# Kernel tuning notes

Measured on AMD Instinct MI355X. Metric: run time of the kernel, lower is better.

## Reference

```python
import jax, jax.numpy as jnp
import numpy as np

DZ, DA, K, T, BS, H = 32, 16, 3, 128, 512, 128


def setup_inputs() -> dict:
    key = jax.random.key(0)
    ks = jax.random.split(key, 8)
    s = 0.02
    # A/C: identity-like init (as in the torch module) plus small noise, per mixture k and timestep t
    A = jnp.eye(DZ, dtype=jnp.float32) + s * jax.random.normal(ks[0], (K, T, DZ, DZ), jnp.float32)
    C = jnp.eye(DA, DZ, dtype=jnp.float32) + s * jax.random.normal(ks[1], (K, T, DA, DZ), jnp.float32)
    a0 = jnp.zeros((DA,), jnp.float32)
    a = jax.random.normal(ks[2], (BS, T, DA), jnp.float32)

    def lw(k, shape):
        return 0.05 * jax.random.normal(k, shape, jnp.float32)

    Wih0 = lw(ks[3], (4 * H, DA)); Whh0 = lw(ks[4], (4 * H, H))
    bih0 = jnp.zeros((4 * H,), jnp.float32); bhh0 = jnp.zeros((4 * H,), jnp.float32)
    Wih1 = lw(ks[5], (4 * H, H)); Whh1 = lw(ks[6], (4 * H, H))
    bih1 = jnp.zeros((4 * H,), jnp.float32); bhh1 = jnp.zeros((4 * H,), jnp.float32)
    Wlin = lw(ks[7], (K, H)); blin = jnp.zeros((K,), jnp.float32)
    return dict(a=a, A=A, C=C, a0=a0, Wih0=Wih0, Whh0=Whh0, bih0=bih0, bhh0=bhh0,
                Wih1=Wih1, Whh1=Whh1, bih1=bih1, bhh1=bhh1, Wlin=Wlin, blin=blin)


def _lstm_layer(x, Wih, Whh, bih, bhh):
    # x: (bs, L, din) -> (bs, L, H); PyTorch gate order i, f, g, o; zero initial state
    Hd = Whh.shape[1]
    b = bih + bhh

    def step(carry, xt):
        h, c = carry
        g = xt @ Wih.T + h @ Whh.T + b
        i, f, gg, o = jnp.split(g, 4, axis=-1)
        c = jax.nn.sigmoid(f) * c + jax.nn.sigmoid(i) * jnp.tanh(gg)
        h = jax.nn.sigmoid(o) * jnp.tanh(c)
        return (h, c), h

    h0 = jnp.zeros((x.shape[0], Hd), x.dtype)
    _, hs = jax.lax.scan(step, (h0, h0), jnp.swapaxes(x, 0, 1))
    return jnp.swapaxes(hs, 0, 1)


def _filter(a, A, C, a0, Wih0, Whh0, bih0, bhh0, Wih1, Whh1, bih1, bhh1, Wlin, blin):
    bs, L, da = a.shape
    dz = A.shape[-1]
    R = 0.01 * jnp.eye(da, dtype=a.dtype)
    Q = 0.01 * jnp.eye(dz, dtype=a.dtype)

    # dynamics network: alpha_t from [a_0, a_0..a_{L-2}]
    code = jnp.concatenate([jnp.broadcast_to(a0, (bs, 1, da)), a[:, :-1]], axis=1)
    h = _lstm_layer(code, Wih0, Whh0, bih0, bhh0)
    h = _lstm_layer(h, Wih1, Whh1, bih1, bhh1)
    alpha = jax.nn.softmax(h @ Wlin.T + blin, axis=-1)  # (bs, L, K)

    A_mix = jnp.einsum('blk,klij->blij', alpha, A)  # (bs, L, dz, dz)
    C_mix = jnp.einsum('blk,klij->blij', alpha, C)  # (bs, L, da, dz)
    # A is applied at index t+1 for the prediction step; last slot is a dummy (its output is unused)
    A_next = jnp.concatenate([A_mix[:, 1:], A_mix[:, -1:]], axis=1)

    mu0 = jnp.zeros((bs, dz), a.dtype)
    sig0 = jnp.broadcast_to(jnp.eye(dz, dtype=a.dtype), (bs, dz, dz))
    I = jnp.eye(dz, dtype=a.dtype)

    def step(carry, inp):
        mu_pred, sigma_pred = carry
        Ct, At_next, at = inp  # (bs,da,dz), (bs,dz,dz), (bs,da)
        r = at - jnp.einsum('bij,bj->bi', Ct, mu_pred)
        CtT = jnp.swapaxes(Ct, 1, 2)
        S = Ct @ sigma_pred @ CtT + R                      # (bs, da, da)
        Kg = sigma_pred @ CtT @ jnp.linalg.inv(S)          # (bs, dz, da)
        mu = mu_pred + jnp.einsum('bij,bj->bi', Kg, r)
        sigma = (I - Kg @ Ct) @ sigma_pred
        mu_next = jnp.einsum('bij,bj->bi', At_next, mu)
        sigma_next = At_next @ sigma @ jnp.swapaxes(At_next, 1, 2) + Q
        return (mu_next, sigma_next), mu

    xs = (jnp.swapaxes(C_mix, 0, 1), jnp.swapaxes(A_next, 0, 1), jnp.swapaxes(a, 0, 1))
    _, means = jax.lax.scan(step, (mu0, sig0), xs)
    return jnp.swapaxes(means, 0, 1)  # filtered means (bs, L, dz)


def reference(a, A, C, a0, Wih0, Whh0, bih0, bhh0, Wih1, Whh1, bih1, bhh1, Wlin, blin):
    return _filter(a, A, C, a0, Wih0, Whh0, bih0, bhh0,
                   Wih1, Whh1, bih1, bhh1, Wlin, blin)
```

## Files before the change

kernel.cpp:

```cpp
#include <hip/hip_runtime.h>
#include <hip/hip_fp16.h>
#include <cstdint>

#define T_LEN 128
#define DA    16
#define DZ    32
#define HH    128

__device__ __forceinline__ float sigm(float x){ return 1.0f/(1.0f + __expf(-x)); }
__device__ __forceinline__ float tanh_f(float x){ return 1.0f - 2.0f/(__expf(2.0f*x)+1.0f); }

typedef _Float16 h2v __attribute__((ext_vector_type(2)));
__device__ __forceinline__ float fdot2(uint32_t w, uint32_t h, float acc){
  union{uint32_t u; h2v v;} a, b; a.u = w; b.u = h;
  return __builtin_amdgcn_fdot2(a.v, b.v, acc, false);
}
__device__ __forceinline__ uint32_t packh2(float x, float y){
  return (uint32_t)__half_as_ushort(__float2half(x)) |
         ((uint32_t)__half_as_ushort(__float2half(y)) << 16);
}
__device__ __forceinline__ float h2lo(uint32_t u){
  return __half2float(__ushort_as_half((unsigned short)(u & 0xffffu)));
}
__device__ __forceinline__ float h2hi(uint32_t u){
  return __half2float(__ushort_as_half((unsigned short)(u >> 16)));
}
__device__ __forceinline__ float dot8(uint4 a, uint4 b, float acc){
  acc = fdot2(a.x, b.x, acc); acc = fdot2(a.y, b.y, acc);
  acc = fdot2(a.z, b.z, acc); acc = fdot2(a.w, b.w, acc);
  return acc;
}
__device__ __forceinline__ float dot8f(uint4 h, float4 f0, float4 f1, float acc){
  acc += h2lo(h.x)*f0.x + h2hi(h.x)*f0.y + h2lo(h.y)*f0.z + h2hi(h.y)*f0.w;
  acc += h2lo(h.z)*f1.x + h2hi(h.z)*f1.y + h2lo(h.w)*f1.z + h2hi(h.w)*f1.w;
  return acc;
}

#define BAR() do { asm volatile("s_waitcnt lgkmcnt(0)" ::: "memory"); \
                   __builtin_amdgcn_s_barrier(); } while (0)

__global__ void prep_kernel(const float* __restrict__ Wih0, const float* __restrict__ Whh0,
                            const float* __restrict__ bih0, const float* __restrict__ bhh0,
                            const float* __restrict__ Wih1, const float* __restrict__ Whh1,
                            const float* __restrict__ bih1, const float* __restrict__ bhh1,
                            uint32_t* __restrict__ ws) {
  int idx = blockIdx.x*256 + threadIdx.x;
  if (idx < 4096) {
    int q = idx & 3, g = (idx >> 2) & 511, m = idx >> 11;
    int k0 = 8*m + 2*q;
    ws[idx] = packh2(Wih0[g*DA + k0], Wih0[g*DA + k0 + 1]);
  } else if (idx < 36864) {
    int f = idx - 4096;
    int q = f & 3, g = (f >> 2) & 511, m = f >> 11;
    int k0 = 8*m + 2*q;
    ws[idx] = packh2(Whh0[g*HH + k0], Whh0[g*HH + k0 + 1]);
  } else if (idx < 69632) {
    int f = idx - 36864;
    int q = f & 3, g = (f >> 2) & 511, m = f >> 11;
    int k0 = 8*m + 2*q;
    ws[idx] = packh2(Wih1[g*HH + k0], Wih1[g*HH + k0 + 1]);
  } else if (idx < 102400) {
    int f = idx - 69632;
    int q = f & 3, g = (f >> 2) & 511, m = f >> 11;
    int k0 = 8*m + 2*q;
    ws[idx] = packh2(Whh1[g*HH + k0], Whh1[g*HH + k0 + 1]);
  } else if (idx < 102912) {
    int j = idx - 102400;
    ((float*)ws)[idx] = bih0[j] + bhh0[j];
  } else if (idx < 103424) {
    int j = idx - 102912;
    ((float*)ws)[idx] = bih1[j] + bhh1[j];
  }
}

__global__ __launch_bounds__(512, 2) void lstm_kernel(
    const float* __restrict__ a, const float* __restrict__ a0,
    const uint32_t* __restrict__ wsw, const float* __restrict__ Wlin,
    const float* __restrict__ blin, float* __restrict__ alpha_out) {
  const uint4* Wih0p = (const uint4*)(wsw);
  const uint4* Whh0p = (const uint4*)(wsw + 4096);
  const uint4* Wih1p = (const uint4*)(wsw + 36864);
  const uint4* Whh1p = (const uint4*)(wsw + 69632);
  const float* b0v = (const float*)(wsw + 102400);
  const float* b1v = (const float*)(wsw + 102912);

  __shared__ __align__(16) uint32_t sxh[2][T_LEN][8];
  __shared__ __align__(16) uint32_t sh0h[2][64];
  __shared__ __align__(16) uint32_t sh1h[2][64];
  __shared__ float gates[2][4*HH];
  __shared__ float hpart[4][3];

  int tid = threadIdx.x;
  int lane = tid & 63;
  int wv = tid >> 6;
  int bb = blockIdx.x * 2;

  uint4 wi0[2], wh0[16], wi1[16], wh1[16];
  #pragma unroll
  for (int m = 0; m < 2; ++m)  wi0[m] = Wih0p[m*512 + tid];
  #pragma unroll
  for (int m = 0; m < 16; ++m) wh0[m] = Whh0p[m*512 + tid];
  #pragma unroll
  for (int m = 0; m < 16; ++m) wi1[m] = Wih1p[m*512 + tid];
  #pragma unroll
  for (int m = 0; m < 16; ++m) wh1[m] = Whh1p[m*512 + tid];
  float bi0 = b0v[tid], bi1 = b1v[tid];

  for (int i = tid; i < 2*T_LEN*8; i += 512) {
    int r = i / (T_LEN*8), rem = i % (T_LEN*8), t = rem >> 3, p = rem & 7;
    float x0, x1;
    if (t == 0) { x0 = a0[2*p]; x1 = a0[2*p+1]; }
    else {
      const float* src = a + ((size_t)(bb + r)*T_LEN + (t-1))*DA;
      x0 = src[2*p]; x1 = src[2*p+1];
    }
    sxh[r][t][p] = packh2(x0, x1);
  }
  float wl0 = Wlin[0*HH + (tid & 127)];
  float wl1 = Wlin[1*HH + (tid & 127)];
  float wl2 = Wlin[2*HH + (tid & 127)];
  float bl0 = blin[0], bl1 = blin[1], bl2 = blin[2];
  float cl0 = 0.f, cl1 = 0.f;
  if (tid < 128) { sh0h[wv][lane] = 0u; sh1h[wv][lane] = 0u; }
  __syncthreads();

  #pragma unroll 1
  for (int t = 0; t < T_LEN; ++t) {
    {
      float g0a = bi0, g0b = 0.f, g1a = bi0, g1b = 0.f;
      uint4 xA0 = *(const uint4*)&sxh[0][t][0];
      uint4 xA1 = *(const uint4*)&sxh[0][t][4];
      uint4 xB0 = *(const uint4*)&sxh[1][t][0];
      uint4 xB1 = *(const uint4*)&sxh[1][t][4];
      g0a = fdot2(wi0[0].x, xA0.x, g0a); g0b = fdot2(wi0[0].y, xA0.y, g0b);
      g0a = fdot2(wi0[0].z, xA0.z, g0a); g0b = fdot2(wi0[0].w, xA0.w, g0b);
      g0a = fdot2(wi0[1].x, xA1.x, g0a); g0b = fdot2(wi0[1].y, xA1.y, g0b);
      g0a = fdot2(wi0[1].z, xA1.z, g0a); g0b = fdot2(wi0[1].w, xA1.w, g0b);
      g1a = fdot2(wi0[0].x, xB0.x, g1a); g1b = fdot2(wi0[0].y, xB0.y, g1b);
      g1a = fdot2(wi0[0].z, xB0.z, g1a); g1b = fdot2(wi0[0].w, xB0.w, g1b);
      g1a = fdot2(wi0[1].x, xB1.x, g1a); g1b = fdot2(wi0[1].y, xB1.y, g1b);
      g1a = fdot2(wi0[1].z, xB1.z, g1a); g1b = fdot2(wi0[1].w, xB1.w, g1b);
      #pragma unroll
      for (int m = 0; m < 16; ++m) {
        uint4 w = wh0[m];
        uint4 hA = *(const uint4*)&sh0h[0][4*m];
        uint4 hB = *(const uint4*)&sh0h[1][4*m];
        g0a = fdot2(w.x, hA.x, g0a); g0b = fdot2(w.y, hA.y, g0b);
        g0a = fdot2(w.z, hA.z, g0a); g0b = fdot2(w.w, hA.w, g0b);
        g1a = fdot2(w.x, hB.x, g1a); g1b = fdot2(w.y, hB.y, g1b);
        g1a = fdot2(w.z, hB.z, g1a); g1b = fdot2(w.w, hB.w, g1b);
      }
      gates[0][tid] = g0a + g0b;
      gates[1][tid] = g1a + g1b;
    }
    __syncthreads();
    if (t > 0 && tid >= 504 && tid < 506) {
      int row = tid - 504;
      float l0 = hpart[2*row][0] + hpart[2*row+1][0] + bl0;
      float l1 = hpart[2*row][1] + hpart[2*row+1][1] + bl1;
      float l2 = hpart[2*row][2] + hpart[2*row+1][2] + bl2;
      float mx = fmaxf(l0, fmaxf(l1, l2));
      float e0=__expf(l0-mx), e1=__expf(l1-mx), e2=__expf(l2-mx);
      float inv = 1.0f/(e0+e1+e2);
      float* dst = alpha_out + (((size_t)(bb+row))*T_LEN + (t-1))*3;
      dst[0]=e0*inv; dst[1]=e1*inv; dst[2]=e2*inv;
    }
    if (tid < 256) {
      int row = tid >> 7, cell = tid & 127;
      float iv = gates[row][cell],      fv = gates[row][cell+HH],
            qv = gates[row][cell+2*HH], ov = gates[row][cell+3*HH];
      cl0 = sigm(fv)*cl0 + sigm(iv)*tanh_f(qv);
      float hv = sigm(ov)*tanh_f(cl0);
      ((__half*)&sh0h[0][0])[row*128 + cell] = __float2half(hv);
    }
    __syncthreads();
    {
      float g0a = bi1, g0b = 0.f, g1a = bi1, g1b = 0.f;
      #pragma unroll
      for (int m = 0; m < 16; ++m) {
        uint4 w = wi1[m];
        uint4 hA = *(const uint4*)&sh0h[0][4*m];
        uint4 hB = *(const uint4*)&sh0h[1][4*m];
        g0a = fdot2(w.x, hA.x, g0a); g0b = fdot2(w.y, hA.y, g0b);
        g0a = fdot2(w.z, hA.z, g0a); g0b = fdot2(w.w, hA.w, g0b);
        g1a = fdot2(w.x, hB.x, g1a); g1b = fdot2(w.y, hB.y, g1b);
        g1a = fdot2(w.z, hB.z, g1a); g1b = fdot2(w.w, hB.w, g1b);
      }
      #pragma unroll
      for (int m = 0; m < 16; ++m) {
        uint4 w = wh1[m];
        uint4 hA = *(const uint4*)&sh1h[0][4*m];
        uint4 hB = *(const uint4*)&sh1h[1][4*m];
        g0a = fdot2(w.x, hA.x, g0a); g0b = fdot2(w.y, hA.y, g0b);
        g0a = fdot2(w.z, hA.z, g0a); g0b = fdot2(w.w, hA.w, g0b);
        g1a = fdot2(w.x, hB.x, g1a); g1b = fdot2(w.y, hB.y, g1b);
        g1a = fdot2(w.z, hB.z, g1a); g1b = fdot2(w.w, hB.w, g1b);
      }
      gates[0][tid] = g0a + g0b;
      gates[1][tid] = g1a + g1b;
    }
    __syncthreads();
    if (tid < 256) {
      int row = tid >> 7, cell = tid & 127;
      float iv = gates[row][cell],      fv = gates[row][cell+HH],
            qv = gates[row][cell+2*HH], ov = gates[row][cell+3*HH];
      cl1 = sigm(fv)*cl1 + sigm(iv)*tanh_f(qv);
      float hv = sigm(ov)*tanh_f(cl1);
      ((__half*)&sh1h[0][0])[row*128 + cell] = __float2half(hv);
      float p0 = hv*wl0, p1 = hv*wl1, p2 = hv*wl2;
      #pragma unroll
      for (int off = 32; off > 0; off >>= 1) {
        p0 += __shfl_down(p0, off); p1 += __shfl_down(p1, off); p2 += __shfl_down(p2, off);
      }
      if (lane == 0) {
        int w4 = tid >> 6;
        hpart[w4][0] = p0; hpart[w4][1] = p1; hpart[w4][2] = p2;
      }
    }
  }
  __syncthreads();
  if (tid >= 504 && tid < 506) {
    int row = tid - 504;
    float l0 = hpart[2*row][0] + hpart[2*row+1][0] + bl0;
    float l1 = hpart[2*row][1] + hpart[2*row+1][1] + bl1;
    float l2 = hpart[2*row][2] + hpart[2*row+1][2] + bl2;
    float mx = fmaxf(l0, fmaxf(l1, l2));
    float e0=__expf(l0-mx), e1=__expf(l1-mx), e2=__expf(l2-mx);
    float inv = 1.0f/(e0+e1+e2);
    float* dst = alpha_out + (((size_t)(bb+row))*T_LEN + (T_LEN-1))*3;
    dst[0]=e0*inv; dst[1]=e1*inv; dst[2]=e2*inv;
  }
}

__global__ __launch_bounds__(256) void kalman_kernel(
    const float* __restrict__ a, const float* __restrict__ A,
    const float* __restrict__ C, const float* __restrict__ alpha,
    float* __restrict__ out) {
  __shared__ __align__(16) uint32_t SgH[DZ][20];
  __shared__ __align__(16) uint32_t AmH[2][DZ][20];
  __shared__ __align__(16) uint32_t CmH[2][DA][20];
  __shared__ __align__(16) uint32_t Sp2H[DZ][20];
  __shared__ __align__(16) uint32_t T2H[DZ][20];
  __shared__ __align__(16) uint32_t NnTH[DA][20];
  __shared__ __align__(16) uint32_t NnH[DZ][12];
  __shared__ __align__(16) uint32_t KgH[DZ][12];
  __shared__ __align__(16) uint32_t SinvH[DA][12];
  __shared__ __align__(16) float Aug[DA][36];
  __shared__ __align__(16) float sa[T_LEN][DA];
  __shared__ float salpha[T_LEN*3];
  __shared__ __align__(16) float muvF[DZ], munF[DZ], rv[DA];

  int tid = threadIdx.x;
  int b = blockIdx.x;

  for (int e = tid; e < T_LEN*DA; e += 256) (&sa[0][0])[e] = a[(size_t)b*T_LEN*DA + e];
  for (int e = tid; e < T_LEN*3; e += 256) salpha[e] = alpha[(size_t)b*T_LEN*3 + e];
  __syncthreads();

  const int i8 = tid >> 3, jq = tid & 7;
  const int i32 = tid & 31, g = tid >> 5;
  const int j2 = g * 2, j4 = g * 4;

  {
    uint2 iv;
    iv.x = packh2((i8==4*jq  )?1.f:0.f, (i8==4*jq+1)?1.f:0.f);
    iv.y = packh2((i8==4*jq+2)?1.f:0.f, (i8==4*jq+3)?1.f:0.f);
    *(uint2*)&SgH[i8][jq*2] = iv;
    if (tid < DZ) muvF[tid] = 0.0f;
  }

  const float4* A4 = (const float4*)A;
  const float4* C4 = (const float4*)C;
  float4 pA0 = A4[(0*T_LEN + 1)*256 + tid];
  float4 pA1 = A4[(1*T_LEN + 1)*256 + tid];
  float4 pA2 = A4[(2*T_LEN + 1)*256 + tid];
  float4 pC0, pC1, pC2;
  if (tid < 128) {
    pC0 = C4[(0*T_LEN + 0)*128 + tid];
    pC1 = C4[(1*T_LEN + 0)*128 + tid];
    pC2 = C4[(2*T_LEN + 0)*128 + tid];
  }
  #define MIX_AND_PREFETCH(bf, s, sn)                                          \
  {                                                                            \
    int ta_ = ((s) < T_LEN-1) ? (s)+1 : (s);                                   \
    float bA0 = salpha[ta_*3+0], bA1 = salpha[ta_*3+1], bA2 = salpha[ta_*3+2]; \
    float bC0 = salpha[(s)*3+0], bC1 = salpha[(s)*3+1], bC2 = salpha[(s)*3+2]; \
    float vx = bA0*pA0.x + bA1*pA1.x + bA2*pA2.x;                              \
    float vy = bA0*pA0.y + bA1*pA1.y + bA2*pA2.y;                              \
    float vz = bA0*pA0.z + bA1*pA1.z + bA2*pA2.z;                              \
    float vw = bA0*pA0.w + bA1*pA1.w + bA2*pA2.w;                              \
    uint2 pv; pv.x = packh2(vx, vy); pv.y = packh2(vz, vw);                    \
    *(uint2*)&AmH[bf][i8][jq*2] = pv;                                          \
    if (tid < 128) {                                                           \
      float cx = bC0*pC0.x + bC1*pC1.x + bC2*pC2.x;                            \
      float cy = bC0*pC0.y + bC1*pC1.y + bC2*pC2.y;                            \
      float cz = bC0*pC0.z + bC1*pC1.z + bC2*pC2.z;                            \
      float cw = bC0*pC0.w + bC1*pC1.w + bC2*pC2.w;                            \
      uint2 pc; pc.x = packh2(cx, cy); pc.y = packh2(cz, cw);                  \
      *(uint2*)&CmH[bf][tid>>3][(tid&7)*2] = pc;                               \
    }                                                                          \
    int sn_ = ((sn) < T_LEN) ? (sn) : T_LEN-1;                                 \
    int tan_ = (sn_ < T_LEN-1) ? sn_+1 : sn_;                                  \
    pA0 = A4[(0*T_LEN + tan_)*256 + tid];                                      \
    pA1 = A4[(1*T_LEN + tan_)*256 + tid];                                      \
    pA2 = A4[(2*T_LEN + tan_)*256 + tid];                                      \
    if (tid < 128) {                                                           \
      pC0 = C4[(0*T_LEN + sn_)*128 + tid];                                     \
      pC1 = C4[(1*T_LEN + sn_)*128 + tid];                                     \
      pC2 = C4[(2*T_LEN + sn_)*128 + tid];                                     \
    }                                                                          \
  }

  MIX_AND_PREFETCH(0, 0, 1)
  __syncthreads();

  #pragma unroll 1
  for (int t = 0; t < T_LEN; ++t) {
    const int p = t & 1;

    {
      uint4 s0 = *(const uint4*)&SgH[i32][0];
      uint4 s1 = *(const uint4*)&SgH[i32][4];
      uint4 s2 = *(const uint4*)&SgH[i32][8];
      uint4 s3 = *(const uint4*)&SgH[i32][12];
      uint4 cA0 = *(const uint4*)&CmH[p][j2][0];
      uint4 cA1 = *(const uint4*)&CmH[p][j2][4];
      uint4 cA2 = *(const uint4*)&CmH[p][j2][8];
      uint4 cA3 = *(const uint4*)&CmH[p][j2][12];
      uint4 cB0 = *(const uint4*)&CmH[p][j2+1][0];
      uint4 cB1 = *(const uint4*)&CmH[p][j2+1][4];
      uint4 cB2 = *(const uint4*)&CmH[p][j2+1][8];
      uint4 cB3 = *(const uint4*)&CmH[p][j2+1][12];
      float aA = dot8(s3,cA3, dot8(s2,cA2, dot8(s1,cA1, dot8(s0,cA0, 0.f))));
      float aB = dot8(s3,cB3, dot8(s2,cB2, dot8(s1,cB1, dot8(s0,cB0, 0.f))));
      NnH[i32][g] = packh2(aA, aB);
      __half* ntp = (__half*)&NnTH[0][0];
      ntp[j2*40 + i32]     = __float2half(aA);
      ntp[(j2+1)*40 + i32] = __float2half(aB);
    }
    BAR();

    {
      int i = tid & 15, j = tid >> 4;
      uint4 c0 = *(const uint4*)&CmH[p][i][0];
      uint4 c1 = *(const uint4*)&CmH[p][i][4];
      uint4 c2 = *(const uint4*)&CmH[p][i][8];
      uint4 c3 = *(const uint4*)&CmH[p][i][12];
      uint4 n0 = *(const uint4*)&NnTH[j][0];
      uint4 n1 = *(const uint4*)&NnTH[j][4];
      uint4 n2 = *(const uint4*)&NnTH[j][8];
      uint4 n3 = *(const uint4*)&NnTH[j][12];
      float s = dot8(c3,n3, dot8(c2,n2, dot8(c1,n1, dot8(c0,n0, 0.f))));
      Aug[i][j] = s + ((i == j) ? 0.01f : 0.0f);
      Aug[i][16 + j] = (i == j) ? 1.0f : 0.0f;
    }
    BAR();

    if (tid < 64) {
      int lane = tid;
      int r = lane >> 2, cb = lane & 3;
      float v[8];
      #pragma unroll
      for (int j = 0; j < 8; ++j) v[j] = Aug[r][cb*8 + j];
      #define GJ_PIVOT(P, CTRL)                                                \
      {                                                                        \
        float App = __int_as_float(__builtin_amdgcn_readlane(                  \
                      __float_as_int(v[(P) & 7]), ((P) << 2) | ((P) >> 3)));   \
        float fv  = __int_as_float(__builtin_amdgcn_mov_dpp(                   \
                      __float_as_int(v[(P) & 7]), (CTRL), 0xf, 0xf, true));    \
        float prow[8];                                                         \
        _Pragma("unroll")                                                      \
        for (int j = 0; j < 8; ++j) prow[j] = __shfl(v[j], ((P) << 2) | cb, 64); \
        float pinv = 1.0f / App;                                               \
        if (r == (P)) {                                                        \
          _Pragma("unroll")                                                    \
          for (int j = 0; j < 8; ++j) v[j] *= pinv;                            \
        } else {                                                               \
          float fp = fv * pinv;                                                \
          _Pragma("unroll")                                                    \
          for (int j = 0; j < 8; ++j) v[j] -= fp * prow[j];                    \
        }                                                                      \
      }
      GJ_PIVOT(0, 0x00)  GJ_PIVOT(1, 0x00)  GJ_PIVOT(2, 0x00)  GJ_PIVOT(3, 0x00)
      GJ_PIVOT(4, 0x00)  GJ_PIVOT(5, 0x00)  GJ_PIVOT(6, 0x00)  GJ_PIVOT(7, 0x00)
      GJ_PIVOT(8, 0x55)  GJ_PIVOT(9, 0x55)  GJ_PIVOT(10, 0x55) GJ_PIVOT(11, 0x55)
      GJ_PIVOT(12, 0x55) GJ_PIVOT(13, 0x55) GJ_PIVOT(14, 0x55) GJ_PIVOT(15, 0x55)
      #undef GJ_PIVOT
      if (cb >= 2) {
        uint4 w;
        w.x = packh2(v[0], v[1]); w.y = packh2(v[2], v[3]);
        w.z = packh2(v[4], v[5]); w.w = packh2(v[6], v[7]);
        *(uint4*)&SinvH[r][(cb-2)*4] = w;
      }
    } else if (tid < 64 + DA) {
      int j = tid - 64;
      uint4 c0 = *(const uint4*)&CmH[p][j][0];
      uint4 c1 = *(const uint4*)&CmH[p][j][4];
      uint4 c2 = *(const uint4*)&CmH[p][j][8];
      uint4 c3 = *(const uint4*)&CmH[p][j][12];
      const float4* mv = (const float4*)muvF;
      float4 m0 = mv[0], m1 = mv[1], m2 = mv[2], m3 = mv[3];
      float4 m4 = mv[4], m5 = mv[5], m6 = mv[6], m7 = mv[7];
      float d = 0.f;
      d = dot8f(c0, m0, m1, d);
      d = dot8f(c1, m2, m3, d);
      d = dot8f(c2, m4, m5, d);
      d = dot8f(c3, m6, m7, d);
      rv[j] = sa[t][j] - d;
    }
    BAR();

    {
      uint4 n0 = *(const uint4*)&NnH[i32][0];
      uint4 n1 = *(const uint4*)&NnH[i32][4];
      uint4 sA0 = *(const uint4*)&SinvH[j2][0];
      uint4 sA1 = *(const uint4*)&SinvH[j2][4];
      uint4 sB0 = *(const uint4*)&SinvH[j2+1][0];
      uint4 sB1 = *(const uint4*)&SinvH[j2+1][4];
      float aA = dot8(n1, sA1, dot8(n0, sA0, 0.f));
      float aB = dot8(n1, sB1, dot8(n0, sB0, 0.f));
      KgH[i32][g] = packh2(aA, aB);
    }
    BAR();

    {
      uint4 k0 = *(const uint4*)&KgH[i32][0];
      uint4 k1 = *(const uint4*)&KgH[i32][4];
      float acc[4];
      #pragma unroll
      for (int c = 0; c < 4; ++c) {
        uint4 b0 = *(const uint4*)&NnH[j4+c][0];
        uint4 b1 = *(const uint4*)&NnH[j4+c][4];
        acc[c] = dot8(k1, b1, dot8(k0, b0, 0.f));
      }
      uint2 sgp = *(const uint2*)&SgH[i32][g*2];
      uint2 o;
      o.x = packh2(h2lo(sgp.x) - acc[0], h2hi(sgp.x) - acc[1]);
      o.y = packh2(h2lo(sgp.y) - acc[2], h2hi(sgp.y) - acc[3]);
      *(uint2*)&Sp2H[i32][g*2] = o;
    }
    if (tid >= 128 && tid < 128 + DZ) {
      int q = tid - 128;
      uint4 k0 = *(const uint4*)&KgH[q][0];
      uint4 k1 = *(const uint4*)&KgH[q][4];
      const float4* rp = (const float4*)rv;
      float4 r0 = rp[0], r1 = rp[1], r2 = rp[2], r3 = rp[3];
      float m = muvF[q];
      m = dot8f(k0, r0, r1, m);
      m = dot8f(k1, r2, r3, m);
      munF[q] = m;
      out[((size_t)b*T_LEN + t)*DZ + q] = m;
    }
    BAR();

    {
      uint4 a0 = *(const uint4*)&AmH[p][i32][0];
      uint4 a1 = *(const uint4*)&AmH[p][i32][4];
      uint4 a2 = *(const uint4*)&AmH[p][i32][8];
      uint4 a3 = *(const uint4*)&AmH[p][i32][12];
      float acc[4];
      #pragma unroll
      for (int c = 0; c < 4; ++c) {
        uint4 p0 = *(const uint4*)&Sp2H[j4+c][0];
        uint4 p1 = *(const uint4*)&Sp2H[j4+c][4];
        uint4 p2 = *(const uint4*)&Sp2H[j4+c][8];
        uint4 p3 = *(const uint4*)&Sp2H[j4+c][12];
        acc[c] = dot8(a3,p3, dot8(a2,p2, dot8(a1,p1, dot8(a0,p0, 0.f))));
      }
      uint2 o; o.x = packh2(acc[0], acc[1]); o.y = packh2(acc[2], acc[3]);
      *(uint2*)&T2H[i32][g*2] = o;
    }
    BAR();

    {
      uint4 t0 = *(const uint4*)&T2H[i32][0];
      uint4 t1 = *(const uint4*)&T2H[i32][4];
      uint4 t2 = *(const uint4*)&T2H[i32][8];
      uint4 t3 = *(const uint4*)&T2H[i32][12];
      float acc[4];
      #pragma unroll
      for (int c = 0; c < 4; ++c) {
        uint4 a0 = *(const uint4*)&AmH[p][j4+c][0];
        uint4 a1 = *(const uint4*)&AmH[p][j4+c][4];
        uint4 a2 = *(const uint4*)&AmH[p][j4+c][8];
        uint4 a3 = *(const uint4*)&AmH[p][j4+c][12];
        acc[c] = dot8(t3,a3, dot8(t2,a2, dot8(t1,a1, dot8(t0,a0, 0.f))));
        if (i32 == j4 + c) acc[c] += 0.01f;
      }
      uint2 o; o.x = packh2(acc[0], acc[1]); o.y = packh2(acc[2], acc[3]);
      *(uint2*)&SgH[i32][g*2] = o;
    }
    if (tid >= 128 && tid < 128 + DZ) {
      int q = tid - 128;
      uint4 a0 = *(const uint4*)&AmH[p][q][0];
      uint4 a1 = *(const uint4*)&AmH[p][q][4];
      uint4 a2 = *(const uint4*)&AmH[p][q][8];
      uint4 a3 = *(const uint4*)&AmH[p][q][12];
      const float4* mp = (const float4*)munF;
      float4 n0 = mp[0], n1 = mp[1], n2 = mp[2], n3 = mp[3];
      float4 n4 = mp[4], n5 = mp[5], n6 = mp[6], n7 = mp[7];
      float m = 0.f;
      m = dot8f(a0, n0, n1, m);
      m = dot8f(a1, n2, n3, m);
      m = dot8f(a2, n4, n5, m);
      m = dot8f(a3, n6, n7, m);
      muvF[q] = m;
    }
    {
      int s = (t+1 < T_LEN) ? t+1 : T_LEN-1;
      MIX_AND_PREFETCH(p^1, s, t+2)
    }
    BAR();
  }
  #undef MIX_AND_PREFETCH
}

extern "C" void kernel_launch(void* const* d_in, const int* in_sizes, int n_in,
                              void* d_out, int out_size, void* d_ws, size_t ws_size,
                              hipStream_t stream) {
  const float* a    = (const float*)d_in[0];
  const float* A    = (const float*)d_in[1];
  const float* C    = (const float*)d_in[2];
  const float* a0   = (const float*)d_in[3];
  const float* Wih0 = (const float*)d_in[4];
  const float* Whh0 = (const float*)d_in[5];
  const float* bih0 = (const float*)d_in[6];
  const float* bhh0 = (const float*)d_in[7];
  const float* Wih1 = (const float*)d_in[8];
  const float* Whh1 = (const float*)d_in[9];
  const float* bih1 = (const float*)d_in[10];
  const float* bhh1 = (const float*)d_in[11];
  const float* Wlin = (const float*)d_in[12];
  const float* blin = (const float*)d_in[13];
  uint32_t* ws = (uint32_t*)d_ws;
  float* alpha = (float*)(ws + 103424);
  float* out = (float*)d_out;

  prep_kernel<<<404, 256, 0, stream>>>(Wih0, Whh0, bih0, bhh0, Wih1, Whh1, bih1, bhh1, ws);
  lstm_kernel<<<256, 512, 0, stream>>>(a, a0, ws, Wlin, blin, alpha);
  kalman_kernel<<<512, 256, 0, stream>>>(a, A, C, alpha, out);
}
```

Before: 1.048 ms.

## Solve S·[Kᵀ|w]=[Nᵀ|r] directly via Gauss-Jordan instead of explicit inverse

```diff
diff --git a/kernel.cpp b/kernel.cpp
--- a/kernel.cpp
+++ b/kernel.cpp
@@ -244,11 +244,10 @@
   __shared__ __align__(16) uint32_t NnTH[DA][20];
   __shared__ __align__(16) uint32_t NnH[DZ][12];
   __shared__ __align__(16) uint32_t KgH[DZ][12];
-  __shared__ __align__(16) uint32_t SinvH[DA][12];
-  __shared__ __align__(16) float Aug[DA][36];
+  __shared__ __align__(16) float Aug[DA][20];
   __shared__ __align__(16) float sa[T_LEN][DA];
   __shared__ float salpha[T_LEN*3];
-  __shared__ __align__(16) float muvF[DZ], munF[DZ], rv[DA];
+  __shared__ __align__(16) float muvF[DZ], munF[DZ], rv[DA], wvF[DA];
 
   int tid = threadIdx.x;
   int b = blockIdx.x;
@@ -337,6 +336,20 @@
       __half* ntp = (__half*)&NnTH[0][0];
       ntp[j2*40 + i32]     = __float2half(aA);
       ntp[(j2+1)*40 + i32] = __float2half(aB);
+      if (tid >= 192 && tid < 192 + DA) {
+        int jr = tid - 192;
+        uint4 d0 = *(const uint4*)&CmH[p][jr][0];
+        uint4 d1 = *(const uint4*)&CmH[p][jr][4];
+        uint4 d2 = *(const uint4*)&CmH[p][jr][8];
+        uint4 d3 = *(const uint4*)&CmH[p][jr][12];
+        const float4* mv = (const float4*)muvF;
+        float d = 0.f;
+        d = dot8f(d0, mv[0], mv[1], d);
+        d = dot8f(d1, mv[2], mv[3], d);
+        d = dot8f(d2, mv[4], mv[5], d);
+        d = dot8f(d3, mv[6], mv[7], d);
+        rv[jr] = sa[t][jr] - d;
+      }
     }
     BAR();
 
@@ -352,74 +365,57 @@
       uint4 n3 = *(const uint4*)&NnTH[j][12];
       float s = dot8(c3,n3, dot8(c2,n2, dot8(c1,n1, dot8(c0,n0, 0.f))));
       Aug[i][j] = s + ((i == j) ? 0.01f : 0.0f);
-      Aug[i][16 + j] = (i == j) ? 1.0f : 0.0f;
     }
     BAR();
 
     if (tid < 64) {
       int lane = tid;
       int r = lane >> 2, cb = lane & 3;
-      float v[8];
-      #pragma unroll
-      for (int j = 0; j < 8; ++j) v[j] = Aug[r][cb*8 + j];
-      #define GJ_PIVOT(P, CTRL)                                                \
+      int base = cb * 13;
+      const __half* ntrow = (const __half*)&NnTH[r][0];
+      float v[13];
+      #pragma unroll
+      for (int k = 0; k < 13; ++k) {
+        int c = base + k;
+        float x = 0.f;
+        if (c < 16) x = Aug[r][c];
+        else if (c < 48) x = __half2float(ntrow[c - 16]);
+        else if (c == 48) x = rv[r];
+        v[k] = x;
+      }
+      #define GJS_PIVOT(P, E, CTRL)                                            \
       {                                                                        \
         float App = __int_as_float(__builtin_amdgcn_readlane(                  \
-                      __float_as_int(v[(P) & 7]), ((P) << 2) | ((P) >> 3)));   \
+                      __float_as_int(v[(E)]), ((P) << 2) | ((P) / 13)));       \
         float fv  = __int_as_float(__builtin_amdgcn_mov_dpp(                   \
-                      __float_as_int(v[(P) & 7]), (CTRL), 0xf, 0xf, true));    \
-        float prow[8];                                                         \
+                      __float_as_int(v[(E)]), (CTRL), 0xf, 0xf, true));        \
+        float prow[13];                                                        \
         _Pragma("unroll")                                                      \
-        for (int j = 0; j < 8; ++j) prow[j] = __shfl(v[j], ((P) << 2) | cb, 64); \
+        for (int j = 0; j < 13; ++j) prow[j] = __shfl(v[j], ((P) << 2) | cb, 64); \
         float pinv = 1.0f / App;                                               \
         if (r == (P)) {                                                        \
           _Pragma("unroll")                                                    \
-          for (int j = 0; j < 8; ++j) v[j] *= pinv;                            \
+          for (int j = 0; j < 13; ++j) v[j] *= pinv;                           \
         } else {                                                               \
           float fp = fv * pinv;                                                \
           _Pragma("unroll")                                                    \
-          for (int j = 0; j < 8; ++j) v[j] -= fp * prow[j];                    \
+          for (int j = 0; j < 13; ++j) v[j] -= fp * prow[j];                   \
         }                                                                      \
       }
-      GJ_PIVOT(0, 0x00)  GJ_PIVOT(1, 0x00)  GJ_PIVOT(2, 0x00)  GJ_PIVOT(3, 0x00)
-      GJ_PIVOT(4, 0x00)  GJ_PIVOT(5, 0x00)  GJ_PIVOT(6, 0x00)  GJ_PIVOT(7, 0x00)
-      GJ_PIVOT(8, 0x55)  GJ_PIVOT(9, 0x55)  GJ_PIVOT(10, 0x55) GJ_PIVOT(11, 0x55)
-      GJ_PIVOT(12, 0x55) GJ_PIVOT(13, 0x55) GJ_PIVOT(14, 0x55) GJ_PIVOT(15, 0x55)
-      #undef GJ_PIVOT
-      if (cb >= 2) {
-        uint4 w;
-        w.x = packh2(v[0], v[1]); w.y = packh2(v[2], v[3]);
-        w.z = packh2(v[4], v[5]); w.w = packh2(v[6], v[7]);
-        *(uint4*)&SinvH[r][(cb-2)*4] = w;
-      }
-    } else if (tid < 64 + DA) {
-      int j = tid - 64;
-      uint4 c0 = *(const uint4*)&CmH[p][j][0];
-      uint4 c1 = *(const uint4*)&CmH[p][j][4];
-      uint4 c2 = *(const uint4*)&CmH[p][j][8];
-      uint4 c3 = *(const uint4*)&CmH[p][j][12];
-      const float4* mv = (const float4*)muvF;
-      float4 m0 = mv[0], m1 = mv[1], m2 = mv[2], m3 = mv[3];
-      float4 m4 = mv[4], m5 = mv[5], m6 = mv[6], m7 = mv[7];
-      float d = 0.f;
-      d = dot8f(c0, m0, m1, d);
-      d = dot8f(c1, m2, m3, d);
-      d = dot8f(c2, m4, m5, d);
-      d = dot8f(c3, m6, m7, d);
-      rv[j] = sa[t][j] - d;
-    }
-    BAR();
-
-    {
-      uint4 n0 = *(const uint4*)&NnH[i32][0];
-      uint4 n1 = *(const uint4*)&NnH[i32][4];
-      uint4 sA0 = *(const uint4*)&SinvH[j2][0];
-      uint4 sA1 = *(const uint4*)&SinvH[j2][4];
-      uint4 sB0 = *(const uint4*)&SinvH[j2+1][0];
-      uint4 sB1 = *(const uint4*)&SinvH[j2+1][4];
-      float aA = dot8(n1, sA1, dot8(n0, sA0, 0.f));
-      float aB = dot8(n1, sB1, dot8(n0, sB0, 0.f));
-      KgH[i32][g] = packh2(aA, aB);
+      GJS_PIVOT(0, 0, 0x00)  GJS_PIVOT(1, 1, 0x00)  GJS_PIVOT(2, 2, 0x00)
+      GJS_PIVOT(3, 3, 0x00)  GJS_PIVOT(4, 4, 0x00)  GJS_PIVOT(5, 5, 0x00)
+      GJS_PIVOT(6, 6, 0x00)  GJS_PIVOT(7, 7, 0x00)  GJS_PIVOT(8, 8, 0x00)
+      GJS_PIVOT(9, 9, 0x00)  GJS_PIVOT(10, 10, 0x00) GJS_PIVOT(11, 11, 0x00)
+      GJS_PIVOT(12, 12, 0x00)
+      GJS_PIVOT(13, 0, 0x55) GJS_PIVOT(14, 1, 0x55) GJS_PIVOT(15, 2, 0x55)
+      #undef GJS_PIVOT
+      __half* kp = (__half*)&KgH[0][0];
+      #pragma unroll
+      for (int k = 0; k < 13; ++k) {
+        int c = base + k;
+        if (c >= 16 && c < 48) kp[(c - 16)*24 + r] = __float2half(v[k]);
+      }
+      if (cb == 3) wvF[r] = v[9];
     }
     BAR();
 
@@ -441,13 +437,12 @@
     }
     if (tid >= 128 && tid < 128 + DZ) {
       int q = tid - 128;
-      uint4 k0 = *(const uint4*)&KgH[q][0];
-      uint4 k1 = *(const uint4*)&KgH[q][4];
-      const float4* rp = (const float4*)rv;
-      float4 r0 = rp[0], r1 = rp[1], r2 = rp[2], r3 = rp[3];
+      uint4 n0 = *(const uint4*)&NnH[q][0];
+      uint4 n1 = *(const uint4*)&NnH[q][4];
+      const float4* wp = (const float4*)wvF;
       float m = muvF[q];
-      m = dot8f(k0, r0, r1, m);
-      m = dot8f(k1, r2, r3, m);
+      m = dot8f(n0, wp[0], wp[1], m);
+      m = dot8f(n1, wp[2], wp[3], m);
       munF[q] = m;
       out[((size_t)b*T_LEN + t)*DZ + q] = m;
     }
@@ -497,13 +492,11 @@
       uint4 a2 = *(const uint4*)&AmH[p][q][8];
       uint4 a3 = *(const uint4*)&AmH[p][q][12];
       const float4* mp = (const float4*)munF;
-      float4 n0 = mp[0], n1 = mp[1], n2 = mp[2], n3 = mp[3];
-      float4 n4 = mp[4], n5 = mp[5], n6 = mp[6], n7 = mp[7];
       float m = 0.f;
-      m = dot8f(a0, n0, n1, m);
-      m = dot8f(a1, n2, n3, m);
-      m = dot8f(a2, n4, n5, m);
-      m = dot8f(a3, n6, n7, m);
+      m = dot8f(a0, mp[0], mp[1], m);
+      m = dot8f(a1, mp[2], mp[3], m);
+      m = dot8f(a2, mp[4], mp[5], m);
+      m = dot8f(a3, mp[6], mp[7], m);
       muvF[q] = m;
     }
     {
```

Result: slower. 1.233 ms (+17.7%).

## Move A/C mixing to idle upper threads and earlier phase of filter step

Applied to the files above, without the earlier changes.

```diff
diff --git a/kernel.cpp b/kernel.cpp
--- a/kernel.cpp
+++ b/kernel.cpp
@@ -271,44 +271,54 @@
 
   const float4* A4 = (const float4*)A;
   const float4* C4 = (const float4*)C;
-  float4 pA0 = A4[(0*T_LEN + 1)*256 + tid];
-  float4 pA1 = A4[(1*T_LEN + 1)*256 + tid];
-  float4 pA2 = A4[(2*T_LEN + 1)*256 + tid];
-  float4 pC0, pC1, pC2;
-  if (tid < 128) {
-    pC0 = C4[(0*T_LEN + 0)*128 + tid];
-    pC1 = C4[(1*T_LEN + 0)*128 + tid];
-    pC2 = C4[(2*T_LEN + 0)*128 + tid];
+  float4 pAl0, pAl1, pAl2, pAh0, pAh1, pAh2, pC0, pC1, pC2;
+  if (tid >= 128) {
+    int u = tid - 128;
+    pAl0 = A4[(0*T_LEN + 1)*256 + u];
+    pAl1 = A4[(1*T_LEN + 1)*256 + u];
+    pAl2 = A4[(2*T_LEN + 1)*256 + u];
+    pAh0 = A4[(0*T_LEN + 1)*256 + u + 128];
+    pAh1 = A4[(1*T_LEN + 1)*256 + u + 128];
+    pAh2 = A4[(2*T_LEN + 1)*256 + u + 128];
+    pC0 = C4[(0*T_LEN + 0)*128 + u];
+    pC1 = C4[(1*T_LEN + 0)*128 + u];
+    pC2 = C4[(2*T_LEN + 0)*128 + u];
   }
   #define MIX_AND_PREFETCH(bf, s, sn)                                          \
-  {                                                                            \
+  if (tid >= 128) {                                                            \
+    int u_ = tid - 128, rl_ = u_ >> 3, q_ = u_ & 7;                            \
     int ta_ = ((s) < T_LEN-1) ? (s)+1 : (s);                                   \
     float bA0 = salpha[ta_*3+0], bA1 = salpha[ta_*3+1], bA2 = salpha[ta_*3+2]; \
     float bC0 = salpha[(s)*3+0], bC1 = salpha[(s)*3+1], bC2 = salpha[(s)*3+2]; \
-    float vx = bA0*pA0.x + bA1*pA1.x + bA2*pA2.x;                              \
-    float vy = bA0*pA0.y + bA1*pA1.y + bA2*pA2.y;                              \
-    float vz = bA0*pA0.z + bA1*pA1.z + bA2*pA2.z;                              \
-    float vw = bA0*pA0.w + bA1*pA1.w + bA2*pA2.w;                              \
+    float vx = bA0*pAl0.x + bA1*pAl1.x + bA2*pAl2.x;                           \
+    float vy = bA0*pAl0.y + bA1*pAl1.y + bA2*pAl2.y;                           \
+    float vz = bA0*pAl0.z + bA1*pAl1.z + bA2*pAl2.z;                           \
+    float vw = bA0*pAl0.w + bA1*pAl1.w + bA2*pAl2.w;                           \
     uint2 pv; pv.x = packh2(vx, vy); pv.y = packh2(vz, vw);                    \
-    *(uint2*)&AmH[bf][i8][jq*2] = pv;                                          \
-    if (tid < 128) {                                                           \
-      float cx = bC0*pC0.x + bC1*pC1.x + bC2*pC2.x;                            \
-      float cy = bC0*pC0.y + bC1*pC1.y + bC2*pC2.y;                            \
-      float cz = bC0*pC0.z + bC1*pC1.z + bC2*pC2.z;                            \
-      float cw = bC0*pC0.w + bC1*pC1.w + bC2*pC2.w;                            \
-      uint2 pc; pc.x = packh2(cx, cy); pc.y = packh2(cz, cw);                  \
-      *(uint2*)&CmH[bf][tid>>3][(tid&7)*2] = pc;                               \
-    }                                                                          \
+    *(uint2*)&AmH[bf][rl_][q_*2] = pv;                                         \
+    vx = bA0*pAh0.x + bA1*pAh1.x + bA2*pAh2.x;                                 \
+    vy = bA0*pAh0.y + bA1*pAh1.y + bA2*pAh2.y;                                 \
+    vz = bA0*pAh0.z + bA1*pAh1.z + bA2*pAh2.z;                                 \
+    vw = bA0*pAh0.w + bA1*pAh1.w + bA2*pAh2.w;                                 \
+    pv.x = packh2(vx, vy); pv.y = packh2(vz, vw);                              \
+    *(uint2*)&AmH[bf][rl_ + 16][q_*2] = pv;                                    \
+    float cx = bC0*pC0.x + bC1*pC1.x + bC2*pC2.x;                              \
+    float cy = bC0*pC0.y + bC1*pC1.y + bC2*pC2.y;                              \
+    float cz = bC0*pC0.z + bC1*pC1.z + bC2*pC2.z;                              \
+    float cw = bC0*pC0.w + bC1*pC1.w + bC2*pC2.w;                              \
+    uint2 pc; pc.x = packh2(cx, cy); pc.y = packh2(cz, cw);                    \
+    *(uint2*)&CmH[bf][rl_][q_*2] = pc;                                         \
     int sn_ = ((sn) < T_LEN) ? (sn) : T_LEN-1;                                 \
     int tan_ = (sn_ < T_LEN-1) ? sn_+1 : sn_;                                  \
-    pA0 = A4[(0*T_LEN + tan_)*256 + tid];                                      \
-    pA1 = A4[(1*T_LEN + tan_)*256 + tid];                                      \
-    pA2 = A4[(2*T_LEN + tan_)*256 + tid];                                      \
-    if (tid < 128) {                                                           \
-      pC0 = C4[(0*T_LEN + sn_)*128 + tid];                                     \
-      pC1 = C4[(1*T_LEN + sn_)*128 + tid];                                     \
-      pC2 = C4[(2*T_LEN + sn_)*128 + tid];                                     \
-    }                                                                          \
+    pAl0 = A4[(0*T_LEN + tan_)*256 + u_];                                      \
+    pAl1 = A4[(1*T_LEN + tan_)*256 + u_];                                      \
+    pAl2 = A4[(2*T_LEN + tan_)*256 + u_];                                      \
+    pAh0 = A4[(0*T_LEN + tan_)*256 + u_ + 128];                                \
+    pAh1 = A4[(1*T_LEN + tan_)*256 + u_ + 128];                                \
+    pAh2 = A4[(2*T_LEN + tan_)*256 + u_ + 128];                                \
+    pC0 = C4[(0*T_LEN + sn_)*128 + u_];                                        \
+    pC1 = C4[(1*T_LEN + sn_)*128 + u_];                                        \
+    pC2 = C4[(2*T_LEN + sn_)*128 + u_];                                        \
   }
 
   MIX_AND_PREFETCH(0, 0, 1)
@@ -408,6 +418,10 @@
       d = dot8f(c3, m6, m7, d);
       rv[j] = sa[t][j] - d;
     }
+    {
+      int s = (t+1 < T_LEN) ? t+1 : T_LEN-1;
+      MIX_AND_PREFETCH(p^1, s, t+2)
+    }
     BAR();
 
     {
@@ -505,10 +519,6 @@
       m = dot8f(a2, n4, n5, m);
       m = dot8f(a3, n6, n7, m);
       muvF[q] = m;
-    }
-    {
-      int s = (t+1 < T_LEN) ? t+1 : T_LEN-1;
-      MIX_AND_PREFETCH(p^1, s, t+2)
     }
     BAR();
   }
```

New measurement: 1.018 ms, median of 2. -2.9%, faster.

## Double Kalman block to 512 threads and move A/C mixing to spare warps

Applied to the files above, without the earlier changes.

```diff
diff --git a/kernel.cpp b/kernel.cpp
--- a/kernel.cpp
+++ b/kernel.cpp
@@ -232,7 +232,7 @@
   }
 }
 
-__global__ __launch_bounds__(256) void kalman_kernel(
+__global__ __launch_bounds__(512, 4) void kalman_kernel(
     const float* __restrict__ a, const float* __restrict__ A,
     const float* __restrict__ C, const float* __restrict__ alpha,
     float* __restrict__ out) {
@@ -253,15 +253,15 @@
   int tid = threadIdx.x;
   int b = blockIdx.x;
 
-  for (int e = tid; e < T_LEN*DA; e += 256) (&sa[0][0])[e] = a[(size_t)b*T_LEN*DA + e];
-  for (int e = tid; e < T_LEN*3; e += 256) salpha[e] = alpha[(size_t)b*T_LEN*3 + e];
+  for (int e = tid; e < T_LEN*DA; e += 512) (&sa[0][0])[e] = a[(size_t)b*T_LEN*DA + e];
+  for (int e = tid; e < T_LEN*3; e += 512) salpha[e] = alpha[(size_t)b*T_LEN*3 + e];
   __syncthreads();
 
-  const int i8 = tid >> 3, jq = tid & 7;
-  const int i32 = tid & 31, g = tid >> 5;
-  const int j2 = g * 2, j4 = g * 4;
-
-  {
+  const int i32 = tid & 31;
+  const int g16 = (tid >> 5) & 15;
+
+  if (tid < 256) {
+    int i8 = tid >> 3, jq = tid & 7;
     uint2 iv;
     iv.x = packh2((i8==4*jq  )?1.f:0.f, (i8==4*jq+1)?1.f:0.f);
     iv.y = packh2((i8==4*jq+2)?1.f:0.f, (i8==4*jq+3)?1.f:0.f);
@@ -271,43 +271,47 @@
 
   const float4* A4 = (const float4*)A;
   const float4* C4 = (const float4*)C;
-  float4 pA0 = A4[(0*T_LEN + 1)*256 + tid];
-  float4 pA1 = A4[(1*T_LEN + 1)*256 + tid];
-  float4 pA2 = A4[(2*T_LEN + 1)*256 + tid];
-  float4 pC0, pC1, pC2;
-  if (tid < 128) {
-    pC0 = C4[(0*T_LEN + 0)*128 + tid];
-    pC1 = C4[(1*T_LEN + 0)*128 + tid];
-    pC2 = C4[(2*T_LEN + 0)*128 + tid];
+  float4 pA0, pA1, pA2, pC0, pC1, pC2;
+  if (tid >= 256) {
+    int u = tid - 256;
+    pA0 = A4[(0*T_LEN + 1)*256 + u];
+    pA1 = A4[(1*T_LEN + 1)*256 + u];
+    pA2 = A4[(2*T_LEN + 1)*256 + u];
+    if (u < 128) {
+      pC0 = C4[(0*T_LEN + 0)*128 + u];
+      pC1 = C4[(1*T_LEN + 0)*128 + u];
+      pC2 = C4[(2*T_LEN + 0)*128 + u];
+    }
   }
   #define MIX_AND_PREFETCH(bf, s, sn)                                          \
-  {                                                                            \
+  if (tid >= 256) {                                                            \
+    int u_ = tid - 256, rl_ = u_ >> 3, q_ = u_ & 7;                            \
     int ta_ = ((s) < T_LEN-1) ? (s)+1 : (s);                                   \
     float bA0 = salpha[ta_*3+0], bA1 = salpha[ta_*3+1], bA2 = salpha[ta_*3+2]; \
-    float bC0 = salpha[(s)*3+0], bC1 = salpha[(s)*3+1], bC2 = salpha[(s)*3+2]; \
     float vx = bA0*pA0.x + bA1*pA1.x + bA2*pA2.x;                              \
     float vy = bA0*pA0.y + bA1*pA1.y + bA2*pA2.y;                              \
     float vz = bA0*pA0.z + bA1*pA1.z + bA2*pA2.z;                              \
     float vw = bA0*pA0.w + bA1*pA1.w + bA2*pA2.w;                              \
     uint2 pv; pv.x = packh2(vx, vy); pv.y = packh2(vz, vw);                    \
-    *(uint2*)&AmH[bf][i8][jq*2] = pv;                                          \
-    if (tid < 128) {                                                           \
+    *(uint2*)&AmH[bf][rl_][q_*2] = pv;                                         \
+    if (u_ < 128) {                                                            \
+      float bC0 = salpha[(s)*3+0], bC1 = salpha[(s)*3+1], bC2 = salpha[(s)*3+2]; \
       float cx = bC0*pC0.x + bC1*pC1.x + bC2*pC2.x;                            \
       float cy = bC0*pC0.y + bC1*pC1.y + bC2*pC2.y;                            \
       float cz = bC0*pC0.z + bC1*pC1.z + bC2*pC2.z;                            \
       float cw = bC0*pC0.w + bC1*pC1.w + bC2*pC2.w;                            \
       uint2 pc; pc.x = packh2(cx, cy); pc.y = packh2(cz, cw);                  \
-      *(uint2*)&CmH[bf][tid>>3][(tid&7)*2] = pc;                               \
+      *(uint2*)&CmH[bf][rl_][q_*2] = pc;                                       \
     }                                                                          \
     int sn_ = ((sn) < T_LEN) ? (sn) : T_LEN-1;                                 \
     int tan_ = (sn_ < T_LEN-1) ? sn_+1 : sn_;                                  \
-    pA0 = A4[(0*T_LEN + tan_)*256 + tid];                                      \
-    pA1 = A4[(1*T_LEN + tan_)*256 + tid];                                      \
-    pA2 = A4[(2*T_LEN + tan_)*256 + tid];                                      \
-    if (tid < 128) {                                                           \
-      pC0 = C4[(0*T_LEN + sn_)*128 + tid];                                     \
-      pC1 = C4[(1*T_LEN + sn_)*128 + tid];                                     \
-      pC2 = C4[(2*T_LEN + sn_)*128 + tid];                                     \
+    pA0 = A4[(0*T_LEN + tan_)*256 + u_];                                       \
+    pA1 = A4[(1*T_LEN + tan_)*256 + u_];                                       \
+    pA2 = A4[(2*T_LEN + tan_)*256 + u_];                                       \
+    if (u_ < 128) {                                                            \
+      pC0 = C4[(0*T_LEN + sn_)*128 + u_];                                      \
+      pC1 = C4[(1*T_LEN + sn_)*128 + u_];                                      \
+      pC2 = C4[(2*T_LEN + sn_)*128 + u_];                                      \
     }                                                                          \
   }
 
@@ -323,24 +327,17 @@
       uint4 s1 = *(const uint4*)&SgH[i32][4];
       uint4 s2 = *(const uint4*)&SgH[i32][8];
       uint4 s3 = *(const uint4*)&SgH[i32][12];
-      uint4 cA0 = *(const uint4*)&CmH[p][j2][0];
-      uint4 cA1 = *(const uint4*)&CmH[p][j2][4];
-      uint4 cA2 = *(const uint4*)&CmH[p][j2][8];
-      uint4 cA3 = *(const uint4*)&CmH[p][j2][12];
-      uint4 cB0 = *(const uint4*)&CmH[p][j2+1][0];
-      uint4 cB1 = *(const uint4*)&CmH[p][j2+1][4];
-      uint4 cB2 = *(const uint4*)&CmH[p][j2+1][8];
-      uint4 cB3 = *(const uint4*)&CmH[p][j2+1][12];
-      float aA = dot8(s3,cA3, dot8(s2,cA2, dot8(s1,cA1, dot8(s0,cA0, 0.f))));
-      float aB = dot8(s3,cB3, dot8(s2,cB2, dot8(s1,cB1, dot8(s0,cB0, 0.f))));
-      NnH[i32][g] = packh2(aA, aB);
-      __half* ntp = (__half*)&NnTH[0][0];
-      ntp[j2*40 + i32]     = __float2half(aA);
-      ntp[(j2+1)*40 + i32] = __float2half(aB);
-    }
-    BAR();
-
-    {
+      uint4 c0 = *(const uint4*)&CmH[p][g16][0];
+      uint4 c1 = *(const uint4*)&CmH[p][g16][4];
+      uint4 c2 = *(const uint4*)&CmH[p][g16][8];
+      uint4 c3 = *(const uint4*)&CmH[p][g16][12];
+      float aA = dot8(s3,c3, dot8(s2,c2, dot8(s1,c1, dot8(s0,c0, 0.f))));
+      ((__half*)&NnH[0][0])[i32*24 + g16] = __float2half(aA);
+      ((__half*)&NnTH[0][0])[g16*40 + i32] = __float2half(aA);
+    }
+    BAR();
+
+    if (tid < 256) {
       int i = tid & 15, j = tid >> 4;
       uint4 c0 = *(const uint4*)&CmH[p][i][0];
       uint4 c1 = *(const uint4*)&CmH[p][i][4];
@@ -353,6 +350,19 @@
       float s = dot8(c3,n3, dot8(c2,n2, dot8(c1,n1, dot8(c0,n0, 0.f))));
       Aug[i][j] = s + ((i == j) ? 0.01f : 0.0f);
       Aug[i][16 + j] = (i == j) ? 1.0f : 0.0f;
+    } else if (tid >= 480 && tid < 480 + DA) {
+      int jr = tid - 480;
+      uint4 c0 = *(const uint4*)&CmH[p][jr][0];
+      uint4 c1 = *(const uint4*)&CmH[p][jr][4];
+      uint4 c2 = *(const uint4*)&CmH[p][jr][8];
+      uint4 c3 = *(const uint4*)&CmH[p][jr][12];
+      const float4* mv = (const float4*)muvF;
+      float d = 0.f;
+      d = dot8f(c0, mv[0], mv[1], d);
+      d = dot8f(c1, mv[2], mv[3], d);
+      d = dot8f(c2, mv[4], mv[5], d);
+      d = dot8f(c3, mv[6], mv[7], d);
+      rv[jr] = sa[t][jr] - d;
     }
     BAR();
 
@@ -392,62 +402,45 @@
         w.z = packh2(v[4], v[5]); w.w = packh2(v[6], v[7]);
         *(uint4*)&SinvH[r][(cb-2)*4] = w;
       }
-    } else if (tid < 64 + DA) {
-      int j = tid - 64;
-      uint4 c0 = *(const uint4*)&CmH[p][j][0];
-      uint4 c1 = *(const uint4*)&CmH[p][j][4];
-      uint4 c2 = *(const uint4*)&CmH[p][j][8];
-      uint4 c3 = *(const uint4*)&CmH[p][j][12];
-      const float4* mv = (const float4*)muvF;
-      float4 m0 = mv[0], m1 = mv[1], m2 = mv[2], m3 = mv[3];
-      float4 m4 = mv[4], m5 = mv[5], m6 = mv[6], m7 = mv[7];
-      float d = 0.f;
-      d = dot8f(c0, m0, m1, d);
-      d = dot8f(c1, m2, m3, d);
-      d = dot8f(c2, m4, m5, d);
-      d = dot8f(c3, m6, m7, d);
-      rv[j] = sa[t][j] - d;
+    }
+    {
+      int s = (t+1 < T_LEN) ? t+1 : T_LEN-1;
+      MIX_AND_PREFETCH(p^1, s, t+2)
     }
     BAR();
 
     {
       uint4 n0 = *(const uint4*)&NnH[i32][0];
       uint4 n1 = *(const uint4*)&NnH[i32][4];
-      uint4 sA0 = *(const uint4*)&SinvH[j2][0];
-      uint4 sA1 = *(const uint4*)&SinvH[j2][4];
-      uint4 sB0 = *(const uint4*)&SinvH[j2+1][0];
-      uint4 sB1 = *(const uint4*)&SinvH[j2+1][4];
-      float aA = dot8(n1, sA1, dot8(n0, sA0, 0.f));
-      float aB = dot8(n1, sB1, dot8(n0, sB0, 0.f));
-      KgH[i32][g] = packh2(aA, aB);
+      uint4 s0 = *(const uint4*)&SinvH[g16][0];
+      uint4 s1 = *(const uint4*)&SinvH[g16][4];
+      float k = dot8(n1, s1, dot8(n0, s0, 0.f));
+      ((__half*)&KgH[0][0])[i32*24 + g16] = __float2half(k);
     }
     BAR();
 
     {
       uint4 k0 = *(const uint4*)&KgH[i32][0];
       uint4 k1 = *(const uint4*)&KgH[i32][4];
-      float acc[4];
-      #pragma unroll
-      for (int c = 0; c < 4; ++c) {
-        uint4 b0 = *(const uint4*)&NnH[j4+c][0];
-        uint4 b1 = *(const uint4*)&NnH[j4+c][4];
+      float acc[2];
+      #pragma unroll
+      for (int c = 0; c < 2; ++c) {
+        uint4 b0 = *(const uint4*)&NnH[2*g16+c][0];
+        uint4 b1 = *(const uint4*)&NnH[2*g16+c][4];
         acc[c] = dot8(k1, b1, dot8(k0, b0, 0.f));
       }
-      uint2 sgp = *(const uint2*)&SgH[i32][g*2];
-      uint2 o;
-      o.x = packh2(h2lo(sgp.x) - acc[0], h2hi(sgp.x) - acc[1]);
-      o.y = packh2(h2lo(sgp.y) - acc[2], h2hi(sgp.y) - acc[3]);
-      *(uint2*)&Sp2H[i32][g*2] = o;
+      uint32_t sgp = SgH[i32][g16];
+      SgH[i32][g16] = sgp;
+      Sp2H[i32][g16] = packh2(h2lo(sgp) - acc[0], h2hi(sgp) - acc[1]);
     }
     if (tid >= 128 && tid < 128 + DZ) {
       int q = tid - 128;
       uint4 k0 = *(const uint4*)&KgH[q][0];
       uint4 k1 = *(const uint4*)&KgH[q][4];
       const float4* rp = (const float4*)rv;
-      float4 r0 = rp[0], r1 = rp[1], r2 = rp[2], r3 = rp[3];
       float m = muvF[q];
-      m = dot8f(k0, r0, r1, m);
-      m = dot8f(k1, r2, r3, m);
+      m = dot8f(k0, rp[0], rp[1], m);
+      m = dot8f(k1, rp[2], rp[3], m);
       munF[q] = m;
       out[((size_t)b*T_LEN + t)*DZ + q] = m;
     }
@@ -458,17 +451,16 @@
       uint4 a1 = *(const uint4*)&AmH[p][i32][4];
       uint4 a2 = *(const uint4*)&AmH[p][i32][8];
       uint4 a3 = *(const uint4*)&AmH[p][i32][12];
-      float acc[4];
-      #pragma unroll
-      for (int c = 0; c < 4; ++c) {
-        uint4 p0 = *(const uint4*)&Sp2H[j4+c][0];
-        uint4 p1 = *(const uint4*)&Sp2H[j4+c][4];
-        uint4 p2 = *(const uint4*)&Sp2H[j4+c][8];
-        uint4 p3 = *(const uint4*)&Sp2H[j4+c][12];
+      float acc[2];
+      #pragma unroll
+      for (int c = 0; c < 2; ++c) {
+        uint4 p0 = *(const uint4*)&Sp2H[2*g16+c][0];
+        uint4 p1 = *(const uint4*)&Sp2H[2*g16+c][4];
+        uint4 p2 = *(const uint4*)&Sp2H[2*g16+c][8];
+        uint4 p3 = *(const uint4*)&Sp2H[2*g16+c][12];
         acc[c] = dot8(a3,p3, dot8(a2,p2, dot8(a1,p1, dot8(a0,p0, 0.f))));
       }
-      uint2 o; o.x = packh2(acc[0], acc[1]); o.y = packh2(acc[2], acc[3]);
-      *(uint2*)&T2H[i32][g*2] = o;
+      T2H[i32][g16] = packh2(acc[0], acc[1]);
     }
     BAR();
 
@@ -477,18 +469,17 @@
       uint4 t1 = *(const uint4*)&T2H[i32][4];
       uint4 t2 = *(const uint4*)&T2H[i32][8];
       uint4 t3 = *(const uint4*)&T2H[i32][12];
-      float acc[4];
-      #pragma unroll
-      for (int c = 0; c < 4; ++c) {
-        uint4 a0 = *(const uint4*)&AmH[p][j4+c][0];
-        uint4 a1 = *(const uint4*)&AmH[p][j4+c][4];
-        uint4 a2 = *(const uint4*)&AmH[p][j4+c][8];
-        uint4 a3 = *(const uint4*)&AmH[p][j4+c][12];
+      float acc[2];
+      #pragma unroll
+      for (int c = 0; c < 2; ++c) {
+        uint4 a0 = *(const uint4*)&AmH[p][2*g16+c][0];
+        uint4 a1 = *(const uint4*)&AmH[p][2*g16+c][4];
+        uint4 a2 = *(const uint4*)&AmH[p][2*g16+c][8];
+        uint4 a3 = *(const uint4*)&AmH[p][2*g16+c][12];
         acc[c] = dot8(t3,a3, dot8(t2,a2, dot8(t1,a1, dot8(t0,a0, 0.f))));
-        if (i32 == j4 + c) acc[c] += 0.01f;
-      }
-      uint2 o; o.x = packh2(acc[0], acc[1]); o.y = packh2(acc[2], acc[3]);
-      *(uint2*)&SgH[i32][g*2] = o;
+        if (i32 == 2*g16 + c) acc[c] += 0.01f;
+      }
+      SgH[i32][g16] = packh2(acc[0], acc[1]);
     }
     if (tid >= 128 && tid < 128 + DZ) {
       int q = tid - 128;
@@ -497,18 +488,12 @@
       uint4 a2 = *(const uint4*)&AmH[p][q][8];
       uint4 a3 = *(const uint4*)&AmH[p][q][12];
       const float4* mp = (const float4*)munF;
-      float4 n0 = mp[0], n1 = mp[1], n2 = mp[2], n3 = mp[3];
-      float4 n4 = mp[4], n5 = mp[5], n6 = mp[6], n7 = mp[7];
       float m = 0.f;
-      m = dot8f(a0, n0, n1, m);
-      m = dot8f(a1, n2, n3, m);
-      m = dot8f(a2, n4, n5, m);
-      m = dot8f(a3, n6, n7, m);
+      m = dot8f(a0, mp[0], mp[1], m);
+      m = dot8f(a1, mp[2], mp[3], m);
+      m = dot8f(a2, mp[4], mp[5], m);
+      m = dot8f(a3, mp[6], mp[7], m);
       muvF[q] = m;
-    }
-    {
-      int s = (t+1 < T_LEN) ? t+1 : T_LEN-1;
-      MIX_AND_PREFETCH(p^1, s, t+2)
     }
     BAR();
   }
@@ -538,5 +523,5 @@
 
   prep_kernel<<<404, 256, 0, stream>>>(Wih0, Whh0, bih0, bhh0, Wih1, Whh1, bih1, bhh1, ws);
   lstm_kernel<<<256, 512, 0, stream>>>(a, a0, ws, Wlin, blin, alpha);
-  kalman_kernel<<<512, 256, 0, stream>>>(a, A, C, alpha, out);
-}
+  kalman_kernel<<<512, 512, 0, stream>>>(a, A, C, alpha, out);
+}
```

New measurement: 1.023 ms. -2.4%, faster.
